# Optimization experiments

Measured on AMD Instinct MI355X. Metric: run time of the kernel, lower is better.

Reference implementation:

```python
import jax, jax.numpy as jnp
import numpy as np

N = 50000      # nodes
E = 800000     # edges (avg degree 16)
F_IN = 256     # input features
H = 128        # hidden
C = 40         # classes


def setup_inputs() -> dict:
    key = jax.random.key(0)
    ks = jax.random.split(key, 10)
    features = jax.random.normal(ks[0], (N, F_IN), dtype=jnp.float32)
    src = jax.random.randint(ks[1], (E,), 0, N, dtype=jnp.int32)
    dst = jax.random.randint(ks[2], (E,), 0, N, dtype=jnp.int32)
    edge_weights = jax.random.uniform(ks[3], (E,), dtype=jnp.float32)
    def glorot(k, i, o):
        return jax.random.normal(k, (i, o), dtype=jnp.float32) * np.float32(1.0 / np.sqrt(i))
    W1 = glorot(ks[4], F_IN, H); b1 = jnp.zeros((H,), jnp.float32)
    W2 = glorot(ks[5], H, H);    b2 = jnp.zeros((H,), jnp.float32)
    W3 = glorot(ks[6], H, C);    b3 = jnp.zeros((C,), jnp.float32)
    return dict(features=features, src=src, dst=dst, edge_weights=edge_weights,
                W1=W1, b1=b1, W2=W2, b2=b2, W3=W3, b3=b3)


def _gcn_layer(h, src, dst, ew, out_norm, in_norm, W, b, act):
    # norm='both': pre-scale by out_degree^-0.5, post-scale by in_degree^-0.5
    h = h * out_norm[:, None]
    in_gt_out = W.shape[0] > W.shape[1]
    if in_gt_out:
        h = h @ W                      # matmul first (in_feats > out_feats)
    # message = u_mul_e, reduce = sum  (SpMM-style gather-scale-scatter)
    agg = jax.ops.segment_sum(h[src] * ew[:, None], dst, num_segments=N)
    if not in_gt_out:
        agg = agg @ W                  # aggregate first (in_feats <= out_feats)
    agg = agg * in_norm[:, None] + b
    return act(agg) if act is not None else agg


def reference(features, src, dst, edge_weights, W1, b1, W2, b2, W3, b3):
    ones = jnp.ones((E,), jnp.float32)
    out_deg = jnp.clip(jax.ops.segment_sum(ones, src, num_segments=N), 1.0)
    in_deg = jnp.clip(jax.ops.segment_sum(ones, dst, num_segments=N), 1.0)
    out_norm = out_deg ** -0.5
    in_norm = in_deg ** -0.5
    relu = jax.nn.relu
    # dropout is identity in eval mode
    h = _gcn_layer(features, src, dst, edge_weights, out_norm, in_norm, W1, b1, relu)
    h = _gcn_layer(h, src, dst, edge_weights, out_norm, in_norm, W2, b2, relu)
    h = _gcn_layer(h, src, dst, edge_weights, out_norm, in_norm, W3, b3, None)
    return h
```

## Files before the change

### kernel.cpp

```cpp
#include <hip/hip_runtime.h>
#include <hip/hip_bf16.h>
#include <cstdint>


#define F_IN 256
#define HDIM 128
#define CDIM 40
#define RBITS 13
#define RSIZE 8192
#define NSUB 64

typedef short bf16x8 __attribute__((ext_vector_type(8)));
typedef float f32x4  __attribute__((ext_vector_type(4)));

__device__ __forceinline__ ushort f2bf(float x) {
    uint b = __float_as_uint(x);
    return (ushort)((b + 0x7fffu + ((b >> 16) & 1u)) >> 16);
}
__device__ __forceinline__ float bf2f(ushort h) {
    return __uint_as_float(((uint)h) << 16);
}

__global__ __launch_bounds__(256)
void histo_range(const int* __restrict__ src, const int* __restrict__ dst,
                 int* __restrict__ pc, int E) {
    __shared__ int h[RSIZE];
    const int s = blockIdx.x;
    const int r = blockIdx.y;
    const int base = r << RBITS;
    const int t = threadIdx.x;
    int4* h4 = reinterpret_cast<int4*>(h);
    for (int j = t; j < RSIZE / 4; j += 256) h4[j] = make_int4(0, 0, 0, 0);
    __syncthreads();

    const int ech = (E + NSUB - 1) / NSUB;
    const int e0 = s * ech;
    const int e1 = min(E, e0 + ech);
    const int n4 = (e1 - e0) >> 2;
    for (int g = t; g < n4; g += 256) {
        int4 d4 = *reinterpret_cast<const int4*>(dst + e0 + g * 4);
        int4 s4 = *reinterpret_cast<const int4*>(src + e0 + g * 4);
        #pragma unroll
        for (int j = 0; j < 4; ++j) {
            int d = (&d4.x)[j] - base;
            int v = (&s4.x)[j] - base;
            if ((unsigned)d < RSIZE) atomicAdd(&h[d], 1);
            if ((unsigned)v < RSIZE) atomicAdd(&h[v], 0x10000);
        }
    }
    for (int e = e0 + n4 * 4 + t; e < e1; e += 256) {
        int d = dst[e] - base, v = src[e] - base;
        if ((unsigned)d < RSIZE) atomicAdd(&h[d], 1);
        if ((unsigned)v < RSIZE) atomicAdd(&h[v], 0x10000);
    }
    __syncthreads();
    int* p = pc + ((size_t)r * NSUB + s) * RSIZE;
    for (int j = t; j < RSIZE; j += 256) p[j] = h[j];
}

__global__ __launch_bounds__(256)
void scan_blocks(const int* __restrict__ pc, int* __restrict__ out,
                 int* __restrict__ bsums, int n) {
    const int t = threadIdx.x;
    const int idx = blockIdx.x * 1024 + t * 4;
    int4 v = make_int4(0, 0, 0, 0);
    if (idx + 3 < n) {
        const int r = idx >> RBITS, off = idx & (RSIZE - 1);
        const int* p = pc + (size_t)r * NSUB * RSIZE + off;
        #pragma unroll 8
        for (int c = 0; c < NSUB; ++c) {
            int4 u = *reinterpret_cast<const int4*>(p + (size_t)c * RSIZE);
            v.x += u.x & 0xffff; v.y += u.y & 0xffff;
            v.z += u.z & 0xffff; v.w += u.w & 0xffff;
        }
    } else {
        for (int j = 0; j < 4; ++j) {
            if (idx + j < n) {
                const int r = (idx + j) >> RBITS, off = (idx + j) & (RSIZE - 1);
                int s = 0;
                for (int c = 0; c < NSUB; ++c)
                    s += pc[(size_t)r * NSUB * RSIZE + (size_t)c * RSIZE + off] & 0xffff;
                (&v.x)[j] = s;
            }
        }
    }
    const int s = v.x + v.y + v.z + v.w;
    const int lane = t & 63;
    int incl = s;
    #pragma unroll
    for (int off = 1; off < 64; off <<= 1) {
        int u = __shfl_up(incl, off);
        if (lane >= off) incl += u;
    }
    __shared__ int wsum[4];
    if (lane == 63) wsum[t >> 6] = incl;
    __syncthreads();
    const int w = t >> 6;
    int woff = 0;
    if (w > 0) woff += wsum[0];
    if (w > 1) woff += wsum[1];
    if (w > 2) woff += wsum[2];
    const int excl = woff + incl - s;
    if (idx + 3 < n) {
        *reinterpret_cast<int4*>(out + idx) =
            make_int4(excl, excl + v.x, excl + v.x + v.y, excl + v.x + v.y + v.z);
    } else {
        if (idx     < n) out[idx]     = excl;
        if (idx + 1 < n) out[idx + 1] = excl + v.x;
        if (idx + 2 < n) out[idx + 2] = excl + v.x + v.y;
        if (idx + 3 < n) out[idx + 3] = excl + v.x + v.y + v.z;
    }
    if (t == 255) bsums[blockIdx.x] = woff + incl;
}

__global__ __launch_bounds__(64)
void scan_sums(int* __restrict__ bsums, int nb) {
    const int lane = threadIdx.x & 63;
    int carry = 0;
    for (int base = 0; base < nb; base += 64) {
        int v = (base + lane < nb) ? bsums[base + lane] : 0;
        int incl = v;
        #pragma unroll
        for (int off = 1; off < 64; off <<= 1) {
            int u = __shfl_up(incl, off);
            if (lane >= off) incl += u;
        }
        if (base + lane < nb) bsums[base + lane] = carry + incl - v;
        carry += __shfl(incl, 63);
    }
}

__global__ __launch_bounds__(256)
void node_prep_kernel(const int* __restrict__ pc,
                      int* __restrict__ row_ptr, const int* __restrict__ bsums,
                      float* __restrict__ out_norm, float* __restrict__ in_norm,
                      int* __restrict__ cb, int n, int E) {
    int i = blockIdx.x * 256 + threadIdx.x;
    if (i < n) {
        const int r = i >> RBITS, off = i & (RSIZE - 1);
        const int* p = pc + (size_t)r * NSUB * RSIZE + off;
        int rp = row_ptr[i] + bsums[i >> 10];
        row_ptr[i] = rp;
        int cur = rp;
        int od = 0;
        #pragma unroll 8
        for (int c = 0; c < NSUB; ++c) {
            unsigned pv = (unsigned)p[(size_t)c * RSIZE];
            cb[(size_t)c * n + i] = cur;
            cur += (int)(pv & 0xffffu);
            od  += (int)(pv >> 16);
        }
        int id = cur - rp;
        out_norm[i] = rsqrtf((float)max(od, 1));
        in_norm[i]  = rsqrtf((float)max(id, 1));
    }
    if (i == 0) row_ptr[n] = E;
}

__global__ __launch_bounds__(256)
void scatter_range(const int* __restrict__ src, const int* __restrict__ dst,
                   const float* __restrict__ ew, const float* __restrict__ out_norm,
                   const int* __restrict__ cb, int2* __restrict__ edges,
                   int E, int N) {
    __shared__ int cur[RSIZE];
    const int s = blockIdx.x;
    const int r = blockIdx.y;
    const int base = r << RBITS;
    const int t = threadIdx.x;
    for (int j = t; j < RSIZE; j += 256)
        if (base + j < N) cur[j] = cb[(size_t)s * N + base + j];
    __syncthreads();

    const int ech = (E + NSUB - 1) / NSUB;
    const int e0 = s * ech;
    const int e1 = min(E, e0 + ech);
    const int n4 = (e1 - e0) >> 2;
    for (int g = t; g < n4; g += 256) {
        int4 d4 = *reinterpret_cast<const int4*>(dst + e0 + g * 4);
        int4 s4 = *reinterpret_cast<const int4*>(src + e0 + g * 4);
        float4 w4 = *reinterpret_cast<const float4*>(ew + e0 + g * 4);
        #pragma unroll
        for (int j = 0; j < 4; ++j) {
            int d = (&d4.x)[j] - base;
            if ((unsigned)d < RSIZE) {
                int sv = (&s4.x)[j];
                int pos = atomicAdd(&cur[d], 1);
                float w = (&w4.x)[j] * out_norm[sv];
                edges[pos] = make_int2(sv, __float_as_int(w));
            }
        }
    }
    for (int e = e0 + n4 * 4 + t; e < e1; e += 256) {
        int d = dst[e] - base;
        if ((unsigned)d < RSIZE) {
            int sv = src[e];
            int pos = atomicAdd(&cur[d], 1);
            float w = ew[e] * out_norm[sv];
            edges[pos] = make_int2(sv, __float_as_int(w));
        }
    }
}

__global__ __launch_bounds__(256)
void conv_w(const float* __restrict__ W, ushort* __restrict__ Wt_hi,
            ushort* __restrict__ Wt_lo, int K) {
    int i = blockIdx.x * 256 + threadIdx.x;
    if (i < K * 128) {
        int k = i >> 7, n = i & 127;
        float x = W[i];
        ushort hi = f2bf(x);
        ushort lo = f2bf(x - bf2f(hi));
        Wt_hi[(size_t)n * K + k] = hi;
        Wt_lo[(size_t)n * K + k] = lo;
    }
}

template <int MODE>
__global__ __launch_bounds__(256)
void gemm128_mfma(const float* __restrict__ A, const ushort* __restrict__ Wt_hi,
                  const ushort* __restrict__ Wt_lo, float* __restrict__ C,
                  int M, int K,
                  const float* __restrict__ rownorm, const float* __restrict__ bias) {
    constexpr int BK = 32;
    constexpr int AP = 40;
    __shared__ __align__(16) ushort As_hi[64 * AP];
    __shared__ __align__(16) ushort As_lo[64 * AP];
    __shared__ __align__(16) ushort Bs_hi[128 * AP];
    __shared__ __align__(16) ushort Bs_lo[128 * AP];

    const int t = threadIdx.x;
    const int w = t >> 6;
    const int l = t & 63;
    const int row0 = blockIdx.x * 64;

    const int ar = t >> 2;
    const int ak = (t & 3) * 8;
    const int bn = t >> 1;
    const int bko = (t & 1) * 16;

    const int fr = l & 15;
    const int fk = (l >> 4) * 8;

    f32x4 acc[8];
    #pragma unroll
    for (int i = 0; i < 8; ++i) acc[i] = (f32x4){0.f, 0.f, 0.f, 0.f};

    const bool arow_ok = (row0 + ar < M);
    const float* ap = A + (size_t)(row0 + ar) * K;

    for (int k0 = 0; k0 < K; k0 += BK) {
        float av[8];
        if (arow_ok) {
            float4 f0 = *reinterpret_cast<const float4*>(ap + k0 + ak);
            float4 f1 = *reinterpret_cast<const float4*>(ap + k0 + ak + 4);
            av[0] = f0.x; av[1] = f0.y; av[2] = f0.z; av[3] = f0.w;
            av[4] = f1.x; av[5] = f1.y; av[6] = f1.z; av[7] = f1.w;
        } else {
            #pragma unroll
            for (int j = 0; j < 8; ++j) av[j] = 0.f;
        }
        bf16x8 ah, al;
        #pragma unroll
        for (int j = 0; j < 8; ++j) {
            ushort hi = f2bf(av[j]);
            ah[j] = (short)hi;
            al[j] = (short)f2bf(av[j] - bf2f(hi));
        }
        const ushort* wh = Wt_hi + (size_t)bn * K + k0 + bko;
        const ushort* wl = Wt_lo + (size_t)bn * K + k0 + bko;
        bf16x8 bh0 = *reinterpret_cast<const bf16x8*>(wh);
        bf16x8 bh1 = *reinterpret_cast<const bf16x8*>(wh + 8);
        bf16x8 bl0 = *reinterpret_cast<const bf16x8*>(wl);
        bf16x8 bl1 = *reinterpret_cast<const bf16x8*>(wl + 8);

        __syncthreads();
        *reinterpret_cast<bf16x8*>(As_hi + ar * AP + ak) = ah;
        *reinterpret_cast<bf16x8*>(As_lo + ar * AP + ak) = al;
        *reinterpret_cast<bf16x8*>(Bs_hi + bn * AP + bko)     = bh0;
        *reinterpret_cast<bf16x8*>(Bs_hi + bn * AP + bko + 8) = bh1;
        *reinterpret_cast<bf16x8*>(Bs_lo + bn * AP + bko)     = bl0;
        *reinterpret_cast<bf16x8*>(Bs_lo + bn * AP + bko + 8) = bl1;
        __syncthreads();

        bf16x8 a_hi = *reinterpret_cast<const bf16x8*>(As_hi + (w * 16 + fr) * AP + fk);
        bf16x8 a_lo = *reinterpret_cast<const bf16x8*>(As_lo + (w * 16 + fr) * AP + fk);
        #pragma unroll
        for (int nt = 0; nt < 8; ++nt) {
            bf16x8 b_hi = *reinterpret_cast<const bf16x8*>(Bs_hi + (nt * 16 + fr) * AP + fk);
            bf16x8 b_lo = *reinterpret_cast<const bf16x8*>(Bs_lo + (nt * 16 + fr) * AP + fk);
            acc[nt] = __builtin_amdgcn_mfma_f32_16x16x32_bf16(a_hi, b_hi, acc[nt], 0, 0, 0);
            acc[nt] = __builtin_amdgcn_mfma_f32_16x16x32_bf16(a_hi, b_lo, acc[nt], 0, 0, 0);
            acc[nt] = __builtin_amdgcn_mfma_f32_16x16x32_bf16(a_lo, b_hi, acc[nt], 0, 0, 0);
        }
    }

    float bb[8];
    if (MODE == 1) {
        #pragma unroll
        for (int nt = 0; nt < 8; ++nt) bb[nt] = bias[nt * 16 + fr];
    }
    #pragma unroll
    for (int r = 0; r < 4; ++r) {
        int row = row0 + w * 16 + (l >> 4) * 4 + r;
        if (row >= M) continue;
        float rn = (MODE == 1) ? rownorm[row] : 0.f;
        float* cp = C + (size_t)row * 128;
        #pragma unroll
        for (int nt = 0; nt < 8; ++nt) {
            float v = acc[nt][r];
            if (MODE == 1) v = fmaxf(fmaf(v, rn, bb[nt]), 0.f);
            cp[nt * 16 + fr] = v;
        }
    }
}

template <int MODE>
__global__ __launch_bounds__(256)
void gemm_f32(const float* __restrict__ A, const float* __restrict__ B,
              float* __restrict__ C, int M, int Nn, int K,
              int lda, int ldb, int ldc,
              const float* __restrict__ rownorm, const float* __restrict__ bias) {
    constexpr int BM = 64, BN = 64, BK = 16;
    __shared__ float As[BK][BM + 4];
    __shared__ float Bs[BK][BN];

    const int t = threadIdx.x;
    const int row0 = blockIdx.x * BM;
    const int col0 = blockIdx.y * BN;
    const int rowbase = (t >> 4) * 4;
    const int colbase = (t & 15) * 4;
    const int ar  = t >> 2;
    const int akq = (t & 3) * 4;
    const int bk  = t >> 4;
    const int bc4 = (t & 15) * 4;

    float acc[4][4];
    #pragma unroll
    for (int i = 0; i < 4; ++i)
        #pragma unroll
        for (int j = 0; j < 4; ++j) acc[i][j] = 0.f;

    const bool arow_ok = (row0 + ar < M);
    const bool bcol_ok = (col0 + bc4 < Nn);
    const float* ap = A + (size_t)(row0 + ar) * lda + akq;

    float4 a0 = make_float4(0.f, 0.f, 0.f, 0.f), bv = a0;
    if (arow_ok) a0 = *reinterpret_cast<const float4*>(ap);
    if (bcol_ok)
        bv = *reinterpret_cast<const float4*>(B + (size_t)bk * ldb + col0 + bc4);

    for (int k0 = 0; k0 < K; k0 += BK) {
        __syncthreads();
        As[akq + 0][ar] = a0.x;
        As[akq + 1][ar] = a0.y;
        As[akq + 2][ar] = a0.z;
        As[akq + 3][ar] = a0.w;
        *reinterpret_cast<float4*>(&Bs[bk][bc4]) = bv;
        __syncthreads();

        if (k0 + BK < K) {
            if (arow_ok) a0 = *reinterpret_cast<const float4*>(ap + k0 + BK);
            if (bcol_ok)
                bv = *reinterpret_cast<const float4*>(B + (size_t)(k0 + BK + bk) * ldb + col0 + bc4);
        }

        #pragma unroll
        for (int kk = 0; kk < BK; ++kk) {
            float4 av  = *reinterpret_cast<const float4*>(&As[kk][rowbase]);
            float4 bv2 = *reinterpret_cast<const float4*>(&Bs[kk][colbase]);
            float a[4] = {av.x, av.y, av.z, av.w};
            float b[4] = {bv2.x, bv2.y, bv2.z, bv2.w};
            #pragma unroll
            for (int i = 0; i < 4; ++i)
                #pragma unroll
                for (int j = 0; j < 4; ++j)
                    acc[i][j] = fmaf(a[i], b[j], acc[i][j]);
        }
    }

    if (col0 + colbase >= Nn) return;
    float4 bb = make_float4(0.f, 0.f, 0.f, 0.f);
    if (MODE == 1) bb = *reinterpret_cast<const float4*>(bias + col0 + colbase);
    #pragma unroll
    for (int i = 0; i < 4; ++i) {
        int row = row0 + rowbase + i;
        if (row >= M) break;
        float4 v = make_float4(acc[i][0], acc[i][1], acc[i][2], acc[i][3]);
        if (MODE == 1) {
            float rn = rownorm[row];
            v.x = fmaxf(fmaf(v.x, rn, bb.x), 0.f);
            v.y = fmaxf(fmaf(v.y, rn, bb.y), 0.f);
            v.z = fmaxf(fmaf(v.z, rn, bb.z), 0.f);
            v.w = fmaxf(fmaf(v.w, rn, bb.w), 0.f);
        }
        *reinterpret_cast<float4*>(C + (size_t)row * ldc + col0 + colbase) = v;
    }
}

template <int EPI>
__global__ __launch_bounds__(256)
void spmm128(const float* __restrict__ H, const int* __restrict__ row_ptr,
             const int2* __restrict__ edges,
             float* __restrict__ out, const float* __restrict__ in_norm,
             const float* __restrict__ bias, int n) {
    int wid  = (blockIdx.x * 256 + threadIdx.x) >> 6;
    int lane = threadIdx.x & 63;
    if (wid >= n) return;
    const int quarter = lane >> 4;
    const int q       = lane & 15;
    int e0 = row_ptr[wid], e1 = row_ptr[wid + 1];
    float4 acc0 = make_float4(0.f, 0.f, 0.f, 0.f);
    float4 acc1 = make_float4(0.f, 0.f, 0.f, 0.f);
    #pragma unroll 2
    for (int e = e0 + quarter; e < e1; e += 4) {
        int2 er = edges[e];
        int   s = er.x;
        float w = __int_as_float(er.y);
        const float* hp = H + (size_t)s * 128 + q * 4;
        float4 v0 = *reinterpret_cast<const float4*>(hp);
        float4 v1 = *reinterpret_cast<const float4*>(hp + 64);
        acc0.x = fmaf(w, v0.x, acc0.x); acc0.y = fmaf(w, v0.y, acc0.y);
        acc0.z = fmaf(w, v0.z, acc0.z); acc0.w = fmaf(w, v0.w, acc0.w);
        acc1.x = fmaf(w, v1.x, acc1.x); acc1.y = fmaf(w, v1.y, acc1.y);
        acc1.z = fmaf(w, v1.z, acc1.z); acc1.w = fmaf(w, v1.w, acc1.w);
    }
    #pragma unroll
    for (int d = 16; d <= 32; d <<= 1) {
        acc0.x += __shfl_xor(acc0.x, d); acc0.y += __shfl_xor(acc0.y, d);
        acc0.z += __shfl_xor(acc0.z, d); acc0.w += __shfl_xor(acc0.w, d);
        acc1.x += __shfl_xor(acc1.x, d); acc1.y += __shfl_xor(acc1.y, d);
        acc1.z += __shfl_xor(acc1.z, d); acc1.w += __shfl_xor(acc1.w, d);
    }
    if (quarter == 0) {
        if (EPI == 1) {
            float nn = in_norm[wid];
            float4 bb0 = *reinterpret_cast<const float4*>(bias + q * 4);
            float4 bb1 = *reinterpret_cast<const float4*>(bias + 64 + q * 4);
            acc0.x = fmaxf(fmaf(acc0.x, nn, bb0.x), 0.f);
            acc0.y = fmaxf(fmaf(acc0.y, nn, bb0.y), 0.f);
            acc0.z = fmaxf(fmaf(acc0.z, nn, bb0.z), 0.f);
            acc0.w = fmaxf(fmaf(acc0.w, nn, bb0.w), 0.f);
            acc1.x = fmaxf(fmaf(acc1.x, nn, bb1.x), 0.f);
            acc1.y = fmaxf(fmaf(acc1.y, nn, bb1.y), 0.f);
            acc1.z = fmaxf(fmaf(acc1.z, nn, bb1.z), 0.f);
            acc1.w = fmaxf(fmaf(acc1.w, nn, bb1.w), 0.f);
        }
        float* op = out + (size_t)wid * 128 + q * 4;
        *reinterpret_cast<float4*>(op)      = acc0;
        *reinterpret_cast<float4*>(op + 64) = acc1;
    }
}

__global__ __launch_bounds__(256)
void spmm40(const float* __restrict__ H, const int* __restrict__ row_ptr,
            const int2* __restrict__ edges,
            float* __restrict__ out, const float* __restrict__ in_norm,
            const float* __restrict__ bias, int n) {
    int wid  = (blockIdx.x * 256 + threadIdx.x) >> 6;
    int lane = threadIdx.x & 63;
    if (wid >= n) return;
    const int quarter = lane >> 4;
    const int q       = lane & 15;
    int e0 = row_ptr[wid], e1 = row_ptr[wid + 1];
    float4 acc = make_float4(0.f, 0.f, 0.f, 0.f);
    #pragma unroll 2
    for (int e = e0 + quarter; e < e1; e += 4) {
        int2 er = edges[e];
        int   s = er.x;
        float w = __int_as_float(er.y);
        float4 v = *reinterpret_cast<const float4*>(H + (size_t)s * 40 + q * 4);
        acc.x = fmaf(w, v.x, acc.x);
        acc.y = fmaf(w, v.y, acc.y);
        acc.z = fmaf(w, v.z, acc.z);
        acc.w = fmaf(w, v.w, acc.w);
    }
    #pragma unroll
    for (int d = 16; d <= 32; d <<= 1) {
        acc.x += __shfl_xor(acc.x, d);
        acc.y += __shfl_xor(acc.y, d);
        acc.z += __shfl_xor(acc.z, d);
        acc.w += __shfl_xor(acc.w, d);
    }
    if (quarter == 0 && q * 4 < CDIM) {
        float nn = in_norm[wid];
        float4 bb = *reinterpret_cast<const float4*>(bias + q * 4);
        acc.x = fmaf(acc.x, nn, bb.x);
        acc.y = fmaf(acc.y, nn, bb.y);
        acc.z = fmaf(acc.z, nn, bb.z);
        acc.w = fmaf(acc.w, nn, bb.w);
        *reinterpret_cast<float4*>(out + (size_t)wid * CDIM + q * 4) = acc;
    }
}


extern "C" void kernel_launch(void* const* d_in, const int* in_sizes, int n_in,
                              void* d_out, int out_size, void* d_ws, size_t ws_size,
                              hipStream_t stream) {
    const float* features = (const float*)d_in[0];
    const int*   src      = (const int*)d_in[1];
    const int*   dst      = (const int*)d_in[2];
    const float* ew       = (const float*)d_in[3];
    const float* W1       = (const float*)d_in[4];
    const float* b1       = (const float*)d_in[5];
    const float* W2       = (const float*)d_in[6];
    const float* b2       = (const float*)d_in[7];
    const float* W3       = (const float*)d_in[8];
    const float* b3       = (const float*)d_in[9];
    float* out = (float*)d_out;

    const int N = in_sizes[0] / F_IN;
    const int E = in_sizes[1];
    const int NR = (N + RSIZE - 1) >> RBITS;

    char* ws = (char*)d_ws;
    size_t off = 0;
    auto alloc = [&](size_t bytes) -> void* {
        void* p = ws + off;
        off += (bytes + 255) & ~(size_t)255;
        return p;
    };
    int*    row_ptr  = (int*)alloc((size_t)(N + 1) * 4);
    float*  out_norm = (float*)alloc((size_t)N * 4);
    float*  in_norm  = (float*)alloc((size_t)N * 4);
    int2*   edges    = (int2*)alloc((size_t)E * 8);
    float*  B0       = (float*)alloc((size_t)N * HDIM * 4);
    float*  B1       = (float*)alloc((size_t)N * HDIM * 4);
    float*  B2       = (float*)alloc((size_t)N * HDIM * 4);
    const int nb     = (N + 1023) / 1024;
    int*    bsums    = (int*)alloc((size_t)nb * 4);
    ushort* Wt1_hi   = (ushort*)alloc((size_t)F_IN * 128 * 2);
    ushort* Wt1_lo   = (ushort*)alloc((size_t)F_IN * 128 * 2);
    ushort* Wt2_hi   = (ushort*)alloc((size_t)HDIM * 128 * 2);
    ushort* Wt2_lo   = (ushort*)alloc((size_t)HDIM * 128 * 2);
    int*    pc       = (int*)B0;
    int*    cb       = (int*)B1;
    (void)ws_size;

    {
        dim3 grid(NSUB, NR);
        histo_range<<<grid, 256, 0, stream>>>(src, dst, pc, E);
    }
    conv_w<<<(F_IN * 128 + 255) / 256, 256, 0, stream>>>(W1, Wt1_hi, Wt1_lo, F_IN);
    conv_w<<<(HDIM * 128 + 255) / 256, 256, 0, stream>>>(W2, Wt2_hi, Wt2_lo, HDIM);
    scan_blocks<<<nb, 256, 0, stream>>>(pc, row_ptr, bsums, N);
    scan_sums<<<1, 64, 0, stream>>>(bsums, nb);
    int ngrid = (N + 255) / 256;
    node_prep_kernel<<<ngrid, 256, 0, stream>>>(pc, row_ptr, bsums,
                                                out_norm, in_norm, cb, N, E);
    {
        dim3 grid(NSUB, NR);
        scatter_range<<<grid, 256, 0, stream>>>(src, dst, ew, out_norm, cb,
                                                edges, E, N);
    }

    const int spmm_grid = (N + 3) / 4;
    const int ggrid = (N + 63) / 64;

    gemm128_mfma<0><<<ggrid, 256, 0, stream>>>(features, Wt1_hi, Wt1_lo, B0,
                                               N, F_IN, nullptr, nullptr);
    spmm128<1><<<spmm_grid, 256, 0, stream>>>(B0, row_ptr, edges, B1, in_norm, b1, N);

    spmm128<0><<<spmm_grid, 256, 0, stream>>>(B1, row_ptr, edges, B2, nullptr, nullptr, N);
    gemm128_mfma<1><<<ggrid, 256, 0, stream>>>(B2, Wt2_hi, Wt2_lo, B0,
                                               N, HDIM, in_norm, b2);

    {
        dim3 grid(ggrid, 1);
        gemm_f32<0><<<grid, 256, 0, stream>>>(B0, W3, B1, N, CDIM, HDIM,
                                              HDIM, CDIM, 40, nullptr, nullptr);
    }
    spmm40<<<spmm_grid, 256, 0, stream>>>(B1, row_ptr, edges, out, in_norm, b3, N);
}
```

Measured before the change: 249.8 us.

## Use split-bf16 MFMA for final 40-column GEMM and widen dst range buckets

```diff
diff --git a/kernel.cpp b/kernel.cpp
--- a/kernel.cpp
+++ b/kernel.cpp
@@ -6,8 +6,8 @@
 #define F_IN 256
 #define HDIM 128
 #define CDIM 40
-#define RBITS 13
-#define RSIZE 8192
+#define RBITS 14
+#define RSIZE 16384
 #define NSUB 64
 
 typedef short bf16x8 __attribute__((ext_vector_type(8)));
@@ -202,16 +202,15 @@
 }
 
 __global__ __launch_bounds__(256)
-void conv_w(const float* __restrict__ W, ushort* __restrict__ Wt_hi,
-            ushort* __restrict__ Wt_lo, int K) {
+void conv_wT(const float* __restrict__ W, ushort* __restrict__ Wt_hi,
+             ushort* __restrict__ Wt_lo, int K, int Nn, int Npad) {
     int i = blockIdx.x * 256 + threadIdx.x;
-    if (i < K * 128) {
-        int k = i >> 7, n = i & 127;
-        float x = W[i];
+    if (i < Npad * K) {
+        int n = i / K, k = i - n * K;
+        float x = (n < Nn) ? W[(size_t)k * Nn + n] : 0.f;
         ushort hi = f2bf(x);
-        ushort lo = f2bf(x - bf2f(hi));
-        Wt_hi[(size_t)n * K + k] = hi;
-        Wt_lo[(size_t)n * K + k] = lo;
+        Wt_hi[i] = hi;
+        Wt_lo[i] = f2bf(x - bf2f(hi));
     }
 }
 
@@ -314,86 +313,98 @@
     }
 }
 
-template <int MODE>
-__global__ __launch_bounds__(256)
-void gemm_f32(const float* __restrict__ A, const float* __restrict__ B,
-              float* __restrict__ C, int M, int Nn, int K,
-              int lda, int ldb, int ldc,
-              const float* __restrict__ rownorm, const float* __restrict__ bias) {
-    constexpr int BM = 64, BN = 64, BK = 16;
-    __shared__ float As[BK][BM + 4];
-    __shared__ float Bs[BK][BN];
+__global__ __launch_bounds__(256)
+void gemm40_mfma(const float* __restrict__ A, const ushort* __restrict__ Wt_hi,
+                 const ushort* __restrict__ Wt_lo, float* __restrict__ C,
+                 int M, int K) {
+    constexpr int BK = 32;
+    constexpr int AP = 40;
+    __shared__ __align__(16) ushort As_hi[64 * AP];
+    __shared__ __align__(16) ushort As_lo[64 * AP];
+    __shared__ __align__(16) ushort Bs_hi[48 * AP];
+    __shared__ __align__(16) ushort Bs_lo[48 * AP];
 
     const int t = threadIdx.x;
-    const int row0 = blockIdx.x * BM;
-    const int col0 = blockIdx.y * BN;
-    const int rowbase = (t >> 4) * 4;
-    const int colbase = (t & 15) * 4;
-    const int ar  = t >> 2;
-    const int akq = (t & 3) * 4;
-    const int bk  = t >> 4;
-    const int bc4 = (t & 15) * 4;
-
-    float acc[4][4];
-    #pragma unroll
-    for (int i = 0; i < 4; ++i)
-        #pragma unroll
-        for (int j = 0; j < 4; ++j) acc[i][j] = 0.f;
+    const int w = t >> 6;
+    const int l = t & 63;
+    const int row0 = blockIdx.x * 64;
+
+    const int ar = t >> 2;
+    const int ak = (t & 3) * 8;
+    const int bn = t >> 1;
+    const int bko = (t & 1) * 16;
+
+    const int fr = l & 15;
+    const int fk = (l >> 4) * 8;
+
+    f32x4 acc[3];
+    #pragma unroll
+    for (int i = 0; i < 3; ++i) acc[i] = (f32x4){0.f, 0.f, 0.f, 0.f};
 
     const bool arow_ok = (row0 + ar < M);
-    const bool bcol_ok = (col0 + bc4 < Nn);
-    const float* ap = A + (size_t)(row0 + ar) * lda + akq;
-
-    float4 a0 = make_float4(0.f, 0.f, 0.f, 0.f), bv = a0;
-    if (arow_ok) a0 = *reinterpret_cast<const float4*>(ap);
-    if (bcol_ok)
-        bv = *reinterpret_cast<const float4*>(B + (size_t)bk * ldb + col0 + bc4);
+    const float* ap = A + (size_t)(row0 + ar) * K;
 
     for (int k0 = 0; k0 < K; k0 += BK) {
+        float av[8];
+        if (arow_ok) {
+            float4 f0 = *reinterpret_cast<const float4*>(ap + k0 + ak);
+            float4 f1 = *reinterpret_cast<const float4*>(ap + k0 + ak + 4);
+            av[0] = f0.x; av[1] = f0.y; av[2] = f0.z; av[3] = f0.w;
+            av[4] = f1.x; av[5] = f1.y; av[6] = f1.z; av[7] = f1.w;
+        } else {
+            #pragma unroll
+            for (int j = 0; j < 8; ++j) av[j] = 0.f;
+        }
+        bf16x8 ah, al;
+        #pragma unroll
+        for (int j = 0; j < 8; ++j) {
+            ushort hi = f2bf(av[j]);
+            ah[j] = (short)hi;
+            al[j] = (short)f2bf(av[j] - bf2f(hi));
+        }
+        bf16x8 bh0, bh1, bl0, bl1;
+        if (bn < 48) {
+            const ushort* wh = Wt_hi + (size_t)bn * K + k0 + bko;
+            const ushort* wl = Wt_lo + (size_t)bn * K + k0 + bko;
+            bh0 = *reinterpret_cast<const bf16x8*>(wh);
+            bh1 = *reinterpret_cast<const bf16x8*>(wh + 8);
+            bl0 = *reinterpret_cast<const bf16x8*>(wl);
+            bl1 = *reinterpret_cast<const bf16x8*>(wl + 8);
+        }
+
         __syncthreads();
-        As[akq + 0][ar] = a0.x;
-        As[akq + 1][ar] = a0.y;
-        As[akq + 2][ar] = a0.z;
-        As[akq + 3][ar] = a0.w;
-        *reinterpret_cast<float4*>(&Bs[bk][bc4]) = bv;
+        *reinterpret_cast<bf16x8*>(As_hi + ar * AP + ak) = ah;
+        *reinterpret_cast<bf16x8*>(As_lo + ar * AP + ak) = al;
+        if (bn < 48) {
+            *reinterpret_cast<bf16x8*>(Bs_hi + bn * AP + bko)     = bh0;
+            *reinterpret_cast<bf16x8*>(Bs_hi + bn * AP + bko + 8) = bh1;
+            *reinterpret_cast<bf16x8*>(Bs_lo + bn * AP + bko)     = bl0;
+            *reinterpret_cast<bf16x8*>(Bs_lo + bn * AP + bko + 8) = bl1;
+        }
         __syncthreads();
 
-        if (k0 + BK < K) {
-            if (arow_ok) a0 = *reinterpret_cast<const float4*>(ap + k0 + BK);
-            if (bcol_ok)
-                bv = *reinterpret_cast<const float4*>(B + (size_t)(k0 + BK + bk) * ldb + col0 + bc4);
-        }
-
-        #pragma unroll
-        for (int kk = 0; kk < BK; ++kk) {
-            float4 av  = *reinterpret_cast<const float4*>(&As[kk][rowbase]);
-            float4 bv2 = *reinterpret_cast<const float4*>(&Bs[kk][colbase]);
-            float a[4] = {av.x, av.y, av.z, av.w};
-            float b[4] = {bv2.x, bv2.y, bv2.z, bv2.w};
-            #pragma unroll
-            for (int i = 0; i < 4; ++i)
-                #pragma unroll
-                for (int j = 0; j < 4; ++j)
-                    acc[i][j] = fmaf(a[i], b[j], acc[i][j]);
-        }
-    }
-
-    if (col0 + colbase >= Nn) return;
-    float4 bb = make_float4(0.f, 0.f, 0.f, 0.f);
-    if (MODE == 1) bb = *reinterpret_cast<const float4*>(bias + col0 + colbase);
-    #pragma unroll
-    for (int i = 0; i < 4; ++i) {
-        int row = row0 + rowbase + i;
-        if (row >= M) break;
-        float4 v = make_float4(acc[i][0], acc[i][1], acc[i][2], acc[i][3]);
-        if (MODE == 1) {
-            float rn = rownorm[row];
-            v.x = fmaxf(fmaf(v.x, rn, bb.x), 0.f);
-            v.y = fmaxf(fmaf(v.y, rn, bb.y), 0.f);
-            v.z = fmaxf(fmaf(v.z, rn, bb.z), 0.f);
-            v.w = fmaxf(fmaf(v.w, rn, bb.w), 0.f);
-        }
-        *reinterpret_cast<float4*>(C + (size_t)row * ldc + col0 + colbase) = v;
+        bf16x8 a_hi = *reinterpret_cast<const bf16x8*>(As_hi + (w * 16 + fr) * AP + fk);
+        bf16x8 a_lo = *reinterpret_cast<const bf16x8*>(As_lo + (w * 16 + fr) * AP + fk);
+        #pragma unroll
+        for (int nt = 0; nt < 3; ++nt) {
+            bf16x8 b_hi = *reinterpret_cast<const bf16x8*>(Bs_hi + (nt * 16 + fr) * AP + fk);
+            bf16x8 b_lo = *reinterpret_cast<const bf16x8*>(Bs_lo + (nt * 16 + fr) * AP + fk);
+            acc[nt] = __builtin_amdgcn_mfma_f32_16x16x32_bf16(a_hi, b_hi, acc[nt], 0, 0, 0);
+            acc[nt] = __builtin_amdgcn_mfma_f32_16x16x32_bf16(a_hi, b_lo, acc[nt], 0, 0, 0);
+            acc[nt] = __builtin_amdgcn_mfma_f32_16x16x32_bf16(a_lo, b_hi, acc[nt], 0, 0, 0);
+        }
+    }
+
+    #pragma unroll
+    for (int r = 0; r < 4; ++r) {
+        int row = row0 + w * 16 + (l >> 4) * 4 + r;
+        if (row >= M) continue;
+        float* cp = C + (size_t)row * CDIM;
+        #pragma unroll
+        for (int nt = 0; nt < 3; ++nt) {
+            int col = nt * 16 + fr;
+            if (col < CDIM) cp[col] = acc[nt][r];
+        }
     }
 }
 
@@ -532,6 +543,8 @@
     ushort* Wt1_lo   = (ushort*)alloc((size_t)F_IN * 128 * 2);
     ushort* Wt2_hi   = (ushort*)alloc((size_t)HDIM * 128 * 2);
     ushort* Wt2_lo   = (ushort*)alloc((size_t)HDIM * 128 * 2);
+    ushort* Wt3_hi   = (ushort*)alloc((size_t)HDIM * 48 * 2);
+    ushort* Wt3_lo   = (ushort*)alloc((size_t)HDIM * 48 * 2);
     int*    pc       = (int*)B0;
     int*    cb       = (int*)B1;
     (void)ws_size;
@@ -540,8 +553,9 @@
         dim3 grid(NSUB, NR);
         histo_range<<<grid, 256, 0, stream>>>(src, dst, pc, E);
     }
-    conv_w<<<(F_IN * 128 + 255) / 256, 256, 0, stream>>>(W1, Wt1_hi, Wt1_lo, F_IN);
-    conv_w<<<(HDIM * 128 + 255) / 256, 256, 0, stream>>>(W2, Wt2_hi, Wt2_lo, HDIM);
+    conv_wT<<<(128 * F_IN + 255) / 256, 256, 0, stream>>>(W1, Wt1_hi, Wt1_lo, F_IN, 128, 128);
+    conv_wT<<<(128 * HDIM + 255) / 256, 256, 0, stream>>>(W2, Wt2_hi, Wt2_lo, HDIM, 128, 128);
+    conv_wT<<<(48 * HDIM + 255) / 256, 256, 0, stream>>>(W3, Wt3_hi, Wt3_lo, HDIM, CDIM, 48);
     scan_blocks<<<nb, 256, 0, stream>>>(pc, row_ptr, bsums, N);
     scan_sums<<<1, 64, 0, stream>>>(bsums, nb);
     int ngrid = (N + 255) / 256;
@@ -564,10 +578,6 @@
     gemm128_mfma<1><<<ggrid, 256, 0, stream>>>(B2, Wt2_hi, Wt2_lo, B0,
                                                N, HDIM, in_norm, b2);
 
-    {
-        dim3 grid(ggrid, 1);
-        gemm_f32<0><<<grid, 256, 0, stream>>>(B0, W3, B1, N, CDIM, HDIM,
-                                              HDIM, CDIM, 40, nullptr, nullptr);
-    }
+    gemm40_mfma<<<ggrid, 256, 0, stream>>>(B0, Wt3_hi, Wt3_lo, B1, N, HDIM);
     spmm40<<<spmm_grid, 256, 0, stream>>>(B1, row_ptr, edges, out, in_norm, b3, N);
 }
```

Measured after the change: 253.1 us. No clear change (+1.3%).
